# Kernel optimization log

Hardware: AMD Instinct MI355X
Metric: run time of the kernel (lower is better)

## Reference

```python
import jax, jax.numpy as jnp
import numpy as np
from jax import lax


def _conv3x3_same(x, w):
    # x: [B,1,H,W], w: [1,1,3,3]; SAME padding (pad=1), stride 1, no bias
    return lax.conv_general_dilated(
        x, w,
        window_strides=(1, 1),
        padding=((1, 1), (1, 1)),
        dimension_numbers=("NCHW", "OIHW", "NCHW"),
    )


def setup_inputs() -> dict:
    key = jax.random.key(0)
    k1, k2, k3 = jax.random.split(key, 3)
    B, H, W = 16, 2048, 2048
    x = jax.random.normal(k1, (B, 1, H, W), dtype=jnp.float32)
    w1 = jax.random.normal(k2, (1, 1, 3, 3), dtype=jnp.float32)
    w2 = jax.random.normal(k3, (1, 1, 3, 3), dtype=jnp.float32)
    return {"x": x, "w1": w1, "w2": w2}


def reference(x, w1, w2):
    # Tiled conv emulation in the torch source is mathematically equivalent to
    # two consecutive SAME-padded 3x3 single-channel convolutions.
    return _conv3x3_same(_conv3x3_same(x, w1), w2)
```

## Files before the change

kernel.cpp:

```cpp
#include <hip/hip_runtime.h>


#define IMG_H 2048
#define IMG_W 2048
#define TILE  64

__global__ __launch_bounds__(256) void conv3x3x2_fused(
    const float* __restrict__ x,
    const float* __restrict__ w1,
    const float* __restrict__ w2,
    float* __restrict__ out,
    int B)
{
    __shared__ __align__(16) float sx[68][72];
    __shared__ __align__(16) float sy[66][68];

    const int tid  = threadIdx.x;
    const int row0 = blockIdx.y * TILE;
    const int col0 = blockIdx.x * TILE;
    const int b    = blockIdx.z;

    float k1[9], k2[9];
#pragma unroll
    for (int i = 0; i < 9; ++i) { k1[i] = w1[i]; k2[i] = w2[i]; }

    const float* xb = x + (size_t)b * IMG_H * IMG_W;

    for (int f = tid; f < 68 * 18; f += 256) {
        int r  = f / 18;
        int c4 = f - r * 18;
        int gr = row0 - 2 + r;
        int gc = col0 - 4 + c4 * 4;
        float4 v;
        if ((unsigned)gr < (unsigned)IMG_H && gc >= 0 && gc + 3 < IMG_W) {
            v = *(const float4*)(xb + (size_t)gr * IMG_W + gc);
        } else {
            const bool rin = (unsigned)gr < (unsigned)IMG_H;
            const float* rp = xb + (size_t)gr * IMG_W;
            v.x = (rin && (unsigned)(gc + 0) < (unsigned)IMG_W) ? rp[gc + 0] : 0.f;
            v.y = (rin && (unsigned)(gc + 1) < (unsigned)IMG_W) ? rp[gc + 1] : 0.f;
            v.z = (rin && (unsigned)(gc + 2) < (unsigned)IMG_W) ? rp[gc + 2] : 0.f;
            v.w = (rin && (unsigned)(gc + 3) < (unsigned)IMG_W) ? rp[gc + 3] : 0.f;
        }
        *(float4*)&sx[r][c4 * 4] = v;
    }
    __syncthreads();

    for (int g = tid; g < 66 * 17; g += 256) {
        int r  = g / 17;
        int cg = g - r * 17;
        float s0 = 0.f, s1 = 0.f, s2 = 0.f, s3 = 0.f;
#pragma unroll
        for (int dr = 0; dr < 3; ++dr) {
            const float* rp = &sx[r + dr][cg * 4];
            float4 a  = *(const float4*)(rp);
            float4 bb = *(const float4*)(rp + 4);
            float x0 = a.z, x1 = a.w, x2 = bb.x, x3 = bb.y, x4 = bb.z, x5 = bb.w;
            float ka = k1[dr * 3 + 0], kb = k1[dr * 3 + 1], kc = k1[dr * 3 + 2];
            s0 += ka * x0 + kb * x1 + kc * x2;
            s1 += ka * x1 + kb * x2 + kc * x3;
            s2 += ka * x2 + kb * x3 + kc * x4;
            s3 += ka * x3 + kb * x4 + kc * x5;
        }
        const int  yr  = row0 + r - 1;
        const bool rin = (unsigned)yr < (unsigned)IMG_H;
        const int  yc0 = col0 + cg * 4 - 1;
        float4 v;
        v.x = (rin && (unsigned)(yc0 + 0) < (unsigned)IMG_W) ? s0 : 0.f;
        v.y = (rin && (unsigned)(yc0 + 1) < (unsigned)IMG_W) ? s1 : 0.f;
        v.z = (rin && (unsigned)(yc0 + 2) < (unsigned)IMG_W) ? s2 : 0.f;
        v.w = (rin && (unsigned)(yc0 + 3) < (unsigned)IMG_W) ? s3 : 0.f;
        *(float4*)&sy[r][cg * 4] = v;
    }
    __syncthreads();

    float* ob = out + (size_t)b * IMG_H * IMG_W;
    for (int g = tid; g < 64 * 16; g += 256) {
        int r  = g >> 4;
        int cg = g & 15;
        float s0 = 0.f, s1 = 0.f, s2 = 0.f, s3 = 0.f;
#pragma unroll
        for (int dr = 0; dr < 3; ++dr) {
            const float* rp = &sy[r + dr][cg * 4];
            float4 a  = *(const float4*)(rp);
            float4 bb = *(const float4*)(rp + 4);
            float y0 = a.x, y1 = a.y, y2 = a.z, y3 = a.w, y4 = bb.x, y5 = bb.y;
            float ka = k2[dr * 3 + 0], kb = k2[dr * 3 + 1], kc = k2[dr * 3 + 2];
            s0 += ka * y0 + kb * y1 + kc * y2;
            s1 += ka * y1 + kb * y2 + kc * y3;
            s2 += ka * y2 + kb * y3 + kc * y4;
            s3 += ka * y3 + kb * y4 + kc * y5;
        }
        float4 o = make_float4(s0, s1, s2, s3);
        *(float4*)(ob + (size_t)(row0 + r) * IMG_W + col0 + cg * 4) = o;
    }
}

extern "C" void kernel_launch(void* const* d_in, const int* in_sizes, int n_in,
                              void* d_out, int out_size, void* d_ws, size_t ws_size,
                              hipStream_t stream) {
    const float* x  = (const float*)d_in[0];
    const float* w1 = (const float*)d_in[1];
    const float* w2 = (const float*)d_in[2];
    float* out = (float*)d_out;
    int B = in_sizes[0] / (IMG_H * IMG_W);
    dim3 grid(IMG_W / TILE, IMG_H / TILE, B);
    conv3x3x2_fused<<<grid, dim3(256, 1, 1), 0, stream>>>(x, w1, w2, out, B);
}
```

Baseline: 480.4 us.

## Replace shared-memory 2D tiles with register row-streaming fused double conv

Replaces the shared-memory 2D tiling (load a halo tile, compute the intermediate conv into LDS, then compute the output) with a column-strip kernel. Each thread owns 4 columns and walks down 64 rows, keeping a sliding window of input rows and intermediate rows in registers. This removes the LDS traffic, the barriers and the redundant halo recompute between tiles. The cost is that neighbouring columns are re-read from global memory by each thread (three float4 loads per row), which relies on cache hits. The grid also shrinks to 2x32xB blocks, which could reduce occupancy and latency hiding.

```diff
diff --git a/kernel.cpp b/kernel.cpp
--- a/kernel.cpp
+++ b/kernel.cpp
@@ -1,99 +1,106 @@
 #include <hip/hip_runtime.h>
 
 
-#define IMG_H 2048
-#define IMG_W 2048
-#define TILE  64
+#define IMG_H  2048
+#define IMG_W  2048
+#define RCHUNK 64
+#define BLOCK  256
 
-__global__ __launch_bounds__(256) void conv3x3x2_fused(
+__global__ __launch_bounds__(BLOCK) void conv3x3x2_stream(
     const float* __restrict__ x,
     const float* __restrict__ w1,
     const float* __restrict__ w2,
     float* __restrict__ out,
     int B)
 {
-    __shared__ __align__(16) float sx[68][72];
-    __shared__ __align__(16) float sy[66][68];
+    const int tid = threadIdx.x;
+    const int gc  = blockIdx.x * (BLOCK * 4) + tid * 4;
+    const int r0  = blockIdx.y * RCHUNK;
+    const int b   = blockIdx.z;
 
-    const int tid  = threadIdx.x;
-    const int row0 = blockIdx.y * TILE;
-    const int col0 = blockIdx.x * TILE;
-    const int b    = blockIdx.z;
+    const float* xb = x   + (size_t)b * IMG_H * IMG_W;
+    float*       ob = out + (size_t)b * IMG_H * IMG_W;
 
     float k1[9], k2[9];
 #pragma unroll
     for (int i = 0; i < 9; ++i) { k1[i] = w1[i]; k2[i] = w2[i]; }
 
-    const float* xb = x + (size_t)b * IMG_H * IMG_W;
+    const bool le = (gc == 0);
+    const bool re = (gc == IMG_W - 4);
 
-    for (int f = tid; f < 68 * 18; f += 256) {
-        int r  = f / 18;
-        int c4 = f - r * 18;
-        int gr = row0 - 2 + r;
-        int gc = col0 - 4 + c4 * 4;
-        float4 v;
-        if ((unsigned)gr < (unsigned)IMG_H && gc >= 0 && gc + 3 < IMG_W) {
-            v = *(const float4*)(xb + (size_t)gr * IMG_W + gc);
-        } else {
-            const bool rin = (unsigned)gr < (unsigned)IMG_H;
-            const float* rp = xb + (size_t)gr * IMG_W;
-            v.x = (rin && (unsigned)(gc + 0) < (unsigned)IMG_W) ? rp[gc + 0] : 0.f;
-            v.y = (rin && (unsigned)(gc + 1) < (unsigned)IMG_W) ? rp[gc + 1] : 0.f;
-            v.z = (rin && (unsigned)(gc + 2) < (unsigned)IMG_W) ? rp[gc + 2] : 0.f;
-            v.w = (rin && (unsigned)(gc + 3) < (unsigned)IMG_W) ? rp[gc + 3] : 0.f;
+    float xr0[8], xr1[8], xnew[8];
+    float yA[6], yB[6], yC[6], yN[6];
+
+#define LOADX(dst, row_)                                                    \
+    {                                                                       \
+        const int _r = (row_);                                              \
+        const float4 _z4 = make_float4(0.f, 0.f, 0.f, 0.f);                 \
+        float4 _va, _vb, _vc;                                               \
+        if ((unsigned)_r < (unsigned)IMG_H) {                               \
+            const float* _rp = xb + (size_t)_r * IMG_W;                     \
+            _vb = *(const float4*)(_rp + gc);                               \
+            _va = le ? _z4 : *(const float4*)(_rp + gc - 4);                \
+            _vc = re ? _z4 : *(const float4*)(_rp + gc + 4);                \
+        } else { _va = _z4; _vb = _z4; _vc = _z4; }                         \
+        dst[0] = _va.z; dst[1] = _va.w;                                     \
+        dst[2] = _vb.x; dst[3] = _vb.y; dst[4] = _vb.z; dst[5] = _vb.w;     \
+        dst[6] = _vc.x; dst[7] = _vc.y;                                     \
+    }
+
+#define COMPY(dst, a_, b_, c_)                                              \
+    {                                                                       \
+        _Pragma("unroll")                                                   \
+        for (int j = 0; j < 6; ++j) {                                       \
+            dst[j] = k1[0]*a_[j] + k1[1]*a_[j+1] + k1[2]*a_[j+2]            \
+                   + k1[3]*b_[j] + k1[4]*b_[j+1] + k1[5]*b_[j+2]            \
+                   + k1[6]*c_[j] + k1[7]*c_[j+1] + k1[8]*c_[j+2];           \
+        }                                                                   \
+        if (le) dst[0] = 0.f;                                               \
+        if (re) dst[5] = 0.f;                                               \
+    }
+
+#define ZERO6(dst) { _Pragma("unroll") for (int _j = 0; _j < 6; ++_j) dst[_j] = 0.f; }
+
+    {
+        float xa[8], xbv[8], xc[8];
+        LOADX(xa,  r0 - 2);
+        LOADX(xbv, r0 - 1);
+        LOADX(xc,  r0);
+        if (r0 >= 1) { COMPY(yA, xa, xbv, xc); } else { ZERO6(yA); }
+        LOADX(xa, r0 + 1);
+        COMPY(yB, xbv, xc, xa);
+        LOADX(xbv, r0 + 2);
+        COMPY(yC, xc, xa, xbv);
+#pragma unroll
+        for (int k = 0; k < 8; ++k) { xr0[k] = xa[k]; xr1[k] = xbv[k]; }
+    }
+
+#pragma unroll 4
+    for (int t = 0; t < RCHUNK; ++t) {
+        const int r = r0 + t;
+
+        LOADX(xnew, r + 3);
+
+        float s[4];
+#pragma unroll
+        for (int i = 0; i < 4; ++i) {
+            s[i] = k2[0]*yA[i] + k2[1]*yA[i+1] + k2[2]*yA[i+2]
+                 + k2[3]*yB[i] + k2[4]*yB[i+1] + k2[5]*yB[i+2]
+                 + k2[6]*yC[i] + k2[7]*yC[i+1] + k2[8]*yC[i+2];
         }
-        *(float4*)&sx[r][c4 * 4] = v;
+        *(float4*)(ob + (size_t)r * IMG_W + gc) = make_float4(s[0], s[1], s[2], s[3]);
+
+        if (r + 2 < IMG_H) { COMPY(yN, xr0, xr1, xnew); } else { ZERO6(yN); }
+
+#pragma unroll
+        for (int j = 0; j < 6; ++j) { yA[j] = yB[j]; yB[j] = yC[j]; yC[j] = yN[j]; }
+#pragma unroll
+        for (int k = 0; k < 8; ++k) { xr0[k] = xr1[k]; xr1[k] = xnew[k]; }
     }
-    __syncthreads();
 
-    for (int g = tid; g < 66 * 17; g += 256) {
-        int r  = g / 17;
-        int cg = g - r * 17;
-        float s0 = 0.f, s1 = 0.f, s2 = 0.f, s3 = 0.f;
-#pragma unroll
-        for (int dr = 0; dr < 3; ++dr) {
-            const float* rp = &sx[r + dr][cg * 4];
-            float4 a  = *(const float4*)(rp);
-            float4 bb = *(const float4*)(rp + 4);
-            float x0 = a.z, x1 = a.w, x2 = bb.x, x3 = bb.y, x4 = bb.z, x5 = bb.w;
-            float ka = k1[dr * 3 + 0], kb = k1[dr * 3 + 1], kc = k1[dr * 3 + 2];
-            s0 += ka * x0 + kb * x1 + kc * x2;
-            s1 += ka * x1 + kb * x2 + kc * x3;
-            s2 += ka * x2 + kb * x3 + kc * x4;
-            s3 += ka * x3 + kb * x4 + kc * x5;
-        }
-        const int  yr  = row0 + r - 1;
-        const bool rin = (unsigned)yr < (unsigned)IMG_H;
-        const int  yc0 = col0 + cg * 4 - 1;
-        float4 v;
-        v.x = (rin && (unsigned)(yc0 + 0) < (unsigned)IMG_W) ? s0 : 0.f;
-        v.y = (rin && (unsigned)(yc0 + 1) < (unsigned)IMG_W) ? s1 : 0.f;
-        v.z = (rin && (unsigned)(yc0 + 2) < (unsigned)IMG_W) ? s2 : 0.f;
-        v.w = (rin && (unsigned)(yc0 + 3) < (unsigned)IMG_W) ? s3 : 0.f;
-        *(float4*)&sy[r][cg * 4] = v;
-    }
-    __syncthreads();
-
-    float* ob = out + (size_t)b * IMG_H * IMG_W;
-    for (int g = tid; g < 64 * 16; g += 256) {
-        int r  = g >> 4;
-        int cg = g & 15;
-        float s0 = 0.f, s1 = 0.f, s2 = 0.f, s3 = 0.f;
-#pragma unroll
-        for (int dr = 0; dr < 3; ++dr) {
-            const float* rp = &sy[r + dr][cg * 4];
-            float4 a  = *(const float4*)(rp);
-            float4 bb = *(const float4*)(rp + 4);
-            float y0 = a.x, y1 = a.y, y2 = a.z, y3 = a.w, y4 = bb.x, y5 = bb.y;
-            float ka = k2[dr * 3 + 0], kb = k2[dr * 3 + 1], kc = k2[dr * 3 + 2];
-            s0 += ka * y0 + kb * y1 + kc * y2;
-            s1 += ka * y1 + kb * y2 + kc * y3;
-            s2 += ka * y2 + kb * y3 + kc * y4;
-            s3 += ka * y3 + kb * y4 + kc * y5;
-        }
-        float4 o = make_float4(s0, s1, s2, s3);
-        *(float4*)(ob + (size_t)(row0 + r) * IMG_W + col0 + cg * 4) = o;
-    }
+#undef LOADX
+#undef COMPY
+#undef ZERO6
 }
 
 extern "C" void kernel_launch(void* const* d_in, const int* in_sizes, int n_in,
@@ -104,6 +111,6 @@
     const float* w2 = (const float*)d_in[2];
     float* out = (float*)d_out;
     int B = in_sizes[0] / (IMG_H * IMG_W);
-    dim3 grid(IMG_W / TILE, IMG_H / TILE, B);
-    conv3x3x2_fused<<<grid, dim3(256, 1, 1), 0, stream>>>(x, w1, w2, out, B);
+    dim3 grid(IMG_W / (BLOCK * 4), IMG_H / RCHUNK, B);
+    conv3x3x2_stream<<<grid, dim3(BLOCK, 1, 1), 0, stream>>>(x, w1, w2, out, B);
 }
```

After: 451.3 us. -6.1%, faster.
